# Kernel optimization log

Hardware: AMD Instinct MI355X
Metric: run time of the kernel (lower is better)

Reference implementation:

```python
import jax, jax.numpy as jnp
import numpy as np

INITIAL_CAPITAL = 500.0
TRANSACTION_COST = 0.0003
TAU = 1.0  # gumbel-softmax temperature
B, S, F = 256, 4096, 64


def setup_inputs() -> dict:
    key = jax.random.key(0)
    ks = jax.random.split(key, 10)
    features = jax.random.normal(ks[0], (B, S, F), dtype=jnp.float32)
    # make columns 1/2 look like vix level / vix change so branches fire
    features = features.at[:, :, 1].set(20.0 + 10.0 * jax.random.uniform(ks[1], (B, S)))
    features = features.at[:, :, 2].set(0.5 * jax.random.normal(ks[2], (B, S)))
    features = features.at[:, :, 3].set(0.01 * jax.random.normal(ks[3], (B, S)))
    return {
        "features": features,
        "feature_weights": jnp.ones((F,), jnp.float32) / F,
        "long_threshold": jnp.float32(0.52),
        "short_threshold": jnp.float32(0.48),
        "base_position_size": jnp.float32(0.8),
        "conviction_scalar": jnp.float32(0.5),
        "vix_impact": jnp.float32(0.2),
        "vix_collapse_threshold": jnp.float32(0.15),
        "vix_spike_threshold": jnp.float32(0.15),
        "gumbel_noise": jax.random.gumbel(ks[4], (S, B, 3), dtype=jnp.float32),
    }


def reference(features, feature_weights, long_threshold, short_threshold,
              base_position_size, conviction_scalar, vix_impact,
              vix_collapse_threshold, vix_spike_threshold, gumbel_noise):
    batch, seq_len, _ = features.shape
    # predictions: sigmoid of feature-weighted sum  [B,S]
    predictions = jax.nn.sigmoid(jnp.einsum('bsf,f->bs', features, feature_weights))
    # time-major per-step inputs [S,B]
    pred_t = predictions.T
    mom_t = features[:, :, 0].T
    vix_t = features[:, :, 1].T
    vch_t = features[:, :, 2].T
    mret_t = features[:, :, 3].T

    def step(carry, x):
        eq, pos = carry  # eq [B], pos [B,3]
        p, v, dv, m, r, g = x
        signal_strength = jnp.abs(p - 0.5) / 0.5
        vix_collapse = (dv < -vix_collapse_threshold) & (v < 30.0)
        vix_spike = (dv > vix_spike_threshold) & (v > 20.0)
        psz = jnp.clip(base_position_size + conviction_scalar * signal_strength, 0.2, 1.0)
        psz = jnp.where(vix_collapse | vix_spike, psz * (1.0 + vix_impact), psz)
        long_pos = ((p >= long_threshold) & (m > 0)) | vix_collapse
        short_pos = ((p <= short_threshold) & (m < 0)) | vix_spike
        logits = jnp.stack([
            jnp.where(long_pos, 1.0, -10.0),
            jnp.where(short_pos, 1.0, -10.0),
            jnp.where(~long_pos & ~short_pos, 1.0, -10.0),
        ], axis=1)  # [B,3]
        probs = jax.nn.softmax((logits + g) / TAU, axis=1)
        strategy_return = psz * (probs[:, 0] - probs[:, 1]) * r
        position_change = jnp.abs(probs - pos).sum(axis=1)
        eq_new = eq * (1.0 + strategy_return - position_change * TRANSACTION_COST)
        return (eq_new, probs), (eq_new, probs, psz)

    eq0 = jnp.full((batch,), INITIAL_CAPITAL, dtype=features.dtype)
    pos0 = jnp.zeros((batch, 3), features.dtype).at[:, 2].set(1.0)
    (_, _), (eq_seq, pos_seq, psz_seq) = jax.lax.scan(
        step, (eq0, pos0), (pred_t, vix_t, vch_t, mom_t, mret_t, gumbel_noise))
    equity = jnp.concatenate([eq0[:, None], eq_seq.T], axis=1)          # [B,S+1]
    positions = jnp.concatenate([pos0[:, None], jnp.swapaxes(pos_seq, 0, 1)], axis=1)  # [B,S+1,3]
    position_sizes = psz_seq[-1]  # last timestep, matching torch loop leak
    return equity, positions, predictions, position_sizes
```

## Files before the change

kernel.cpp:

```cpp
#include <hip/hip_runtime.h>

#define Bn 256
#define Sn 4096
#define Fn 64
#define TCOST 0.0003f
#define INIT_CAP 500.0f

#define EQ_OFF   0
#define POS_OFF  (Bn * (Sn + 1))
#define PRED_OFF (Bn * (Sn + 1) * 4)
#define PSZ_OFF  (PRED_OFF + Bn * Sn)

__global__ __launch_bounds__(256) void trishot_fwd(
    const float* __restrict__ feat,
    const float* __restrict__ w,
    const float* __restrict__ p_lt, const float* __restrict__ p_st,
    const float* __restrict__ p_bps, const float* __restrict__ p_cs,
    const float* __restrict__ p_vi, const float* __restrict__ p_vct,
    const float* __restrict__ p_vst,
    const float* __restrict__ gumbel,
    float* __restrict__ out)
{
    int r = blockIdx.x * 256 + threadIdx.x;
    int b = r >> 12;
    int s = r & (Sn - 1);

    const float LT = *p_lt, ST = *p_st, BPS = *p_bps, CS = *p_cs,
                VI = *p_vi, VCT = *p_vct, VST = *p_vst;

    const float4* f4 = (const float4*)(feat + (size_t)r * Fn);
    const float4* w4 = (const float4*)w;

    float4 f0 = f4[0];
    float a0 = 0.f, a1 = 0.f, a2 = 0.f, a3 = 0.f;
#pragma unroll
    for (int k = 0; k < 16; k++) {
        float4 fv = f4[k];
        float4 wv = w4[k];
        a0 = fmaf(fv.x, wv.x, a0);
        a1 = fmaf(fv.y, wv.y, a1);
        a2 = fmaf(fv.z, wv.z, a2);
        a3 = fmaf(fv.w, wv.w, a3);
    }
    float x = (a0 + a1) + (a2 + a3);
    float p = 1.0f / (1.0f + __expf(-x));

    float mom = f0.x, vix = f0.y, dvix = f0.z, mret = f0.w;

    float ss = fabsf(p - 0.5f) * 2.0f;
    bool collapse = (dvix < -VCT) && (vix < 30.0f);
    bool spike    = (dvix >  VST) && (vix > 20.0f);
    float psz = fminf(fmaxf(BPS + CS * ss, 0.2f), 1.0f);
    if (collapse || spike) psz *= (1.0f + VI);

    bool lp = ((p >= LT) && (mom > 0.0f)) || collapse;
    bool sp = ((p <= ST) && (mom < 0.0f)) || spike;
    float l0 = lp ? 1.0f : -10.0f;
    float l1 = sp ? 1.0f : -10.0f;
    float l2 = (!lp && !sp) ? 1.0f : -10.0f;

    const float* g = gumbel + ((size_t)s * Bn + b) * 3;
    float g0 = g[0], g1 = g[1], g2 = g[2];
    float z0 = l0 + g0, z1 = l1 + g1, z2 = l2 + g2;
    float zm = fmaxf(z0, fmaxf(z1, z2));
    float e0 = __expf(z0 - zm), e1 = __expf(z1 - zm), e2 = __expf(z2 - zm);
    float inv = 1.0f / (e0 + e1 + e2);
    float q0 = e0 * inv, q1 = e1 * inv, q2 = e2 * inv;

    out[PRED_OFF + r] = p;

    size_t prow = ((size_t)b * (Sn + 1) + s + 1) * 3;
    float* pos = out + POS_OFF;
    pos[prow + 0] = q0;
    pos[prow + 1] = q1;
    pos[prow + 2] = q2;

    out[EQ_OFF + (size_t)b * (Sn + 1) + s + 1] = psz * (q0 - q1) * mret;

    if (s == 0) {
        size_t p0row = (size_t)b * (Sn + 1) * 3;
        pos[p0row + 0] = 0.0f;
        pos[p0row + 1] = 0.0f;
        pos[p0row + 2] = 1.0f;
    }
    if (s == Sn - 1) {
        out[PSZ_OFF + b] = psz;
    }
}

#define CH 16
__global__ __launch_bounds__(256) void trishot_scan(float* __restrict__ out)
{
    int b = blockIdx.x;
    int j = threadIdx.x;

    float* eq = out + EQ_OFF + (size_t)b * (Sn + 1);
    const float* pos = out + POS_OFF + (size_t)b * (Sn + 1) * 3;

    int t0 = j * CH;
    float prev0 = pos[(size_t)t0 * 3 + 0];
    float prev1 = pos[(size_t)t0 * 3 + 1];
    float prev2 = pos[(size_t)t0 * 3 + 2];

    float f[CH];
    float lprod = 1.0f;
#pragma unroll
    for (int i = 0; i < CH; i++) {
        size_t ci = (size_t)(t0 + i + 1) * 3;
        float c0 = pos[ci + 0], c1 = pos[ci + 1], c2 = pos[ci + 2];
        float pc = fabsf(c0 - prev0) + fabsf(c1 - prev1) + fabsf(c2 - prev2);
        float rp = eq[t0 + i + 1];
        float fac = 1.0f + rp - pc * TCOST;
        f[i] = fac;
        lprod *= fac;
        prev0 = c0; prev1 = c1; prev2 = c2;
    }

    __shared__ float sc[256];
    sc[j] = lprod;
    __syncthreads();
#pragma unroll
    for (int off = 1; off < 256; off <<= 1) {
        float mine = sc[j];
        float other = (j >= off) ? sc[j - off] : 1.0f;
        __syncthreads();
        sc[j] = mine * other;
        __syncthreads();
    }

    float eqv = INIT_CAP * ((j > 0) ? sc[j - 1] : 1.0f);
#pragma unroll
    for (int i = 0; i < CH; i++) {
        eqv *= f[i];
        eq[t0 + i + 1] = eqv;
    }
    if (j == 0) eq[0] = INIT_CAP;
}

extern "C" void kernel_launch(void* const* d_in, const int* in_sizes, int n_in,
                              void* d_out, int out_size, void* d_ws, size_t ws_size,
                              hipStream_t stream) {
    const float* feat   = (const float*)d_in[0];
    const float* w      = (const float*)d_in[1];
    const float* lt     = (const float*)d_in[2];
    const float* st     = (const float*)d_in[3];
    const float* bps    = (const float*)d_in[4];
    const float* cs     = (const float*)d_in[5];
    const float* vi     = (const float*)d_in[6];
    const float* vct    = (const float*)d_in[7];
    const float* vst    = (const float*)d_in[8];
    const float* gumbel = (const float*)d_in[9];
    float* out = (float*)d_out;

    trishot_fwd<<<(Bn * Sn) / 256, 256, 0, stream>>>(
        feat, w, lt, st, bps, cs, vi, vct, vst, gumbel, out);
    trishot_scan<<<Bn, 256, 0, stream>>>(out);
}
```

Baseline: 395.1 us.

## Coalesce feature loads with 16-lane row dots and pre-transpose gumbel noise

The forward kernel now has 16 lanes cooperatively load one 256-byte feature row as float4s and reduce the dot product with shuffles, so global reads are coalesced instead of each thread streaming its own row. Per-row results and the first four feature columns are staged through shared memory. A new kernel transposes the gumbel noise from [S,B,3] to [B,S,3] in the workspace so the forward kernel reads it contiguously. The cost is an extra launch plus a full read and write of the 12 MB noise tensor.

```diff
diff --git a/kernel.cpp b/kernel.cpp
--- a/kernel.cpp
+++ b/kernel.cpp
@@ -10,6 +10,30 @@
 #define POS_OFF  (Bn * (Sn + 1))
 #define PRED_OFF (Bn * (Sn + 1) * 4)
 #define PSZ_OFF  (PRED_OFF + Bn * Sn)
+
+__global__ __launch_bounds__(256) void gumbel_transpose(
+    const float* __restrict__ gin,
+    float* __restrict__ gout)
+{
+    __shared__ float tile[32 * 97];
+    int s0 = (blockIdx.x & 127) * 32;
+    int b0 = (blockIdx.x >> 7) * 32;
+
+    for (int idx = threadIdx.x; idx < 32 * 96; idx += 256) {
+        int i = idx / 96;
+        int rem = idx - i * 96;
+        tile[i * 97 + rem] = gin[(size_t)(s0 + i) * (Bn * 3) + b0 * 3 + rem];
+    }
+    __syncthreads();
+    for (int idx = threadIdx.x; idx < 32 * 96; idx += 256) {
+        int j = idx / 96;
+        int rem = idx - j * 96;
+        int i = rem / 3;
+        int c = rem - i * 3;
+        gout[(size_t)(b0 + j) * (Sn * 3) + (size_t)(s0 + i) * 3 + c] =
+            tile[i * 97 + j * 3 + c];
+    }
+}
 
 __global__ __launch_bounds__(256) void trishot_fwd(
     const float* __restrict__ feat,
@@ -18,34 +42,51 @@
     const float* __restrict__ p_bps, const float* __restrict__ p_cs,
     const float* __restrict__ p_vi, const float* __restrict__ p_vct,
     const float* __restrict__ p_vst,
-    const float* __restrict__ gumbel,
+    const float* __restrict__ gt,
     float* __restrict__ out)
 {
-    int r = blockIdx.x * 256 + threadIdx.x;
+    __shared__ float xs[256];
+    __shared__ float m0s[256], v0s[256], d0s[256], r0s[256];
+
+    int t = threadIdx.x;
+    int R0 = blockIdx.x * 256;
+    int g = t >> 4;
+    int l = t & 15;
+
+    float4 wv = ((const float4*)w)[l];
+
+#pragma unroll
+    for (int q = 0; q < 16; q++) {
+        int row = R0 + q * 16 + g;
+        float4 fv = ((const float4*)feat)[(size_t)row * 16 + l];
+        float partial = fmaf(fv.x, wv.x,
+                        fmaf(fv.y, wv.y,
+                        fmaf(fv.z, wv.z, fv.w * wv.w)));
+        partial += __shfl_xor(partial, 1, 64);
+        partial += __shfl_xor(partial, 2, 64);
+        partial += __shfl_xor(partial, 4, 64);
+        partial += __shfl_xor(partial, 8, 64);
+        if (l == 0) {
+            int rr = q * 16 + g;
+            xs[rr]  = partial;
+            m0s[rr] = fv.x;
+            v0s[rr] = fv.y;
+            d0s[rr] = fv.z;
+            r0s[rr] = fv.w;
+        }
+    }
+    __syncthreads();
+
+    int r = R0 + t;
     int b = r >> 12;
     int s = r & (Sn - 1);
 
     const float LT = *p_lt, ST = *p_st, BPS = *p_bps, CS = *p_cs,
                 VI = *p_vi, VCT = *p_vct, VST = *p_vst;
 
-    const float4* f4 = (const float4*)(feat + (size_t)r * Fn);
-    const float4* w4 = (const float4*)w;
-
-    float4 f0 = f4[0];
-    float a0 = 0.f, a1 = 0.f, a2 = 0.f, a3 = 0.f;
-#pragma unroll
-    for (int k = 0; k < 16; k++) {
-        float4 fv = f4[k];
-        float4 wv = w4[k];
-        a0 = fmaf(fv.x, wv.x, a0);
-        a1 = fmaf(fv.y, wv.y, a1);
-        a2 = fmaf(fv.z, wv.z, a2);
-        a3 = fmaf(fv.w, wv.w, a3);
-    }
-    float x = (a0 + a1) + (a2 + a3);
+    float x = xs[t];
     float p = 1.0f / (1.0f + __expf(-x));
-
-    float mom = f0.x, vix = f0.y, dvix = f0.z, mret = f0.w;
+    float mom = m0s[t], vix = v0s[t], dvix = d0s[t], mret = r0s[t];
 
     float ss = fabsf(p - 0.5f) * 2.0f;
     bool collapse = (dvix < -VCT) && (vix < 30.0f);
@@ -59,8 +100,8 @@
     float l1 = sp ? 1.0f : -10.0f;
     float l2 = (!lp && !sp) ? 1.0f : -10.0f;
 
-    const float* g = gumbel + ((size_t)s * Bn + b) * 3;
-    float g0 = g[0], g1 = g[1], g2 = g[2];
+    const float* gg = gt + (size_t)r * 3;
+    float g0 = gg[0], g1 = gg[1], g2 = gg[2];
     float z0 = l0 + g0, z1 = l1 + g1, z2 = l2 + g2;
     float zm = fmaxf(z0, fmaxf(z1, z2));
     float e0 = __expf(z0 - zm), e1 = __expf(z1 - zm), e2 = __expf(z2 - zm);
@@ -151,8 +192,10 @@
     const float* vst    = (const float*)d_in[8];
     const float* gumbel = (const float*)d_in[9];
     float* out = (float*)d_out;
-
+    float* gt  = (float*)d_ws;
+
+    gumbel_transpose<<<128 * 8, 256, 0, stream>>>(gumbel, gt);
     trishot_fwd<<<(Bn * Sn) / 256, 256, 0, stream>>>(
-        feat, w, lt, st, bps, cs, vi, vct, vst, gumbel, out);
+        feat, w, lt, st, bps, cs, vi, vct, vst, gt, out);
     trishot_scan<<<Bn, 256, 0, stream>>>(out);
 }
```

Result: no change. 402.1 us (+1.8%).
